# Kernel optimization log

Hardware: AMD Instinct MI355X
Metric: run time of the kernel (lower is better)

The kernel has to match this reference:

```python
import jax, jax.numpy as jnp
import numpy as np

SMOOTHING = 0.9  # NEURON_CONFIG['signal_smoothing']
NUM_SOURCE = 16384
NUM_TARGET = 16384
NUM_BRANCHES = 64
BATCH = 32


def setup_inputs() -> dict:
    key = jax.random.key(0)
    k1, k2, k3, k4 = jax.random.split(key, 4)
    spikes = jax.random.normal(k1, (BATCH, NUM_SOURCE), dtype=jnp.float32)
    attenuation = jax.random.uniform(k2, (NUM_SOURCE, NUM_BRANCHES), dtype=jnp.float32)
    target_indices = jax.random.randint(k3, (NUM_SOURCE, NUM_BRANCHES), 0, NUM_TARGET)
    delays = jax.random.randint(k4, (NUM_SOURCE, NUM_BRANCHES), 0, 6)
    return {"spikes": spikes, "attenuation": attenuation,
            "target_indices": target_indices, "delays": delays}


def reference(spikes, attenuation, target_indices, delays):
    # spikes: [B, S]; attenuation/delays/target_indices: [S, Br]
    B = spikes.shape[0]
    num_target = NUM_TARGET
    att = jnp.clip(attenuation, 0.0, 1.0)
    decay = SMOOTHING ** delays.astype(spikes.dtype)          # [S, Br]
    # fused elementwise: signal per (batch, source, branch)
    signals = spikes[:, :, None] * (att * decay)[None, :, :]   # [B, S, Br]
    flat_t = target_indices.reshape(-1)                        # [S*Br]
    flat_s = signals.reshape(B, -1)                            # [B, S*Br]
    out = jnp.zeros((B, num_target), dtype=spikes.dtype)
    out = out.at[jnp.arange(B)[:, None], flat_t[None, :]].add(flat_s)
    return out
```

## Files before the change

kernel.cpp:

```cpp
#include <hip/hip_runtime.h>

#define S_   16384
#define T_   16384
#define B_   32
#define NEDGES (S_ * 64)
#define GP_  256
#define EPG  4096
#define NBKT 512
#define TPB  32
#define CAP_SRT 2560

__device__ __forceinline__ float edge_weight(float a, int d) {
  float w = fminf(fmaxf(a, 0.0f), 1.0f);
  float r = (d & 1) ? 0.9f : 1.0f;
  r = (d & 2) ? r * 0.81f   : r;
  r = (d & 4) ? r * 0.6561f : r;
  return w * r;
}

__global__ __launch_bounds__(1024) void produce(
    const float* __restrict__ spikes,
    const float* __restrict__ att,
    const int*   __restrict__ tgt,
    const int*   __restrict__ del,
    float*        __restrict__ spikesT,
    int2*         __restrict__ rec,
    unsigned int* __restrict__ ofse) {
  __shared__ float tile[64][33];
  __shared__ int4  sbuf4[EPG / 2];
  __shared__ int   cnt5[NBKT], cur5[NBKT], sofs5[NBKT];
  __shared__ int   wtot[8];
  int2* buf = (int2*)sbuf4;

  const int g   = blockIdx.x;
  const int tid = threadIdx.x;
  if (tid < NBKT) cnt5[tid] = 0;

  const int s0 = g * 64;
  {
    const int x = tid & 63, y = tid >> 6;
    tile[x][y]      = spikes[(size_t)y        * S_ + s0 + x];
    tile[x][y + 16] = spikes[(size_t)(y + 16) * S_ + s0 + x];
  }

  const int e4  = g * 1024 + tid;
  int4   t = reinterpret_cast<const int4*>(tgt)[e4];
  float4 a = reinterpret_cast<const float4*>(att)[e4];
  int4   d = reinterpret_cast<const int4*>(del)[e4];
  const int src = (e4 * 4) >> 6;

  __syncthreads();

  {
    const int b = tid & 31, j = tid >> 5;
    spikesT[(size_t)(s0 + j)      * 32 + b] = tile[j][b];
    spikesT[(size_t)(s0 + j + 32) * 32 + b] = tile[j + 32][b];
  }

  const int bk0 = t.x >> 5, bk1 = t.y >> 5, bk2 = t.z >> 5, bk3 = t.w >> 5;
  __hip_atomic_fetch_add(&cnt5[bk0], 1, __ATOMIC_RELAXED, __HIP_MEMORY_SCOPE_WORKGROUP);
  __hip_atomic_fetch_add(&cnt5[bk1], 1, __ATOMIC_RELAXED, __HIP_MEMORY_SCOPE_WORKGROUP);
  __hip_atomic_fetch_add(&cnt5[bk2], 1, __ATOMIC_RELAXED, __HIP_MEMORY_SCOPE_WORKGROUP);
  __hip_atomic_fetch_add(&cnt5[bk3], 1, __ATOMIC_RELAXED, __HIP_MEMORY_SCOPE_WORKGROUP);
  __syncthreads();

  int v = 0, incl = 0;
  if (tid < NBKT) {
    v = cnt5[tid];
    incl = v;
#pragma unroll
    for (int off = 1; off < 64; off <<= 1) {
      int u = __shfl_up(incl, off);
      if ((tid & 63) >= off) incl += u;
    }
    if ((tid & 63) == 63) wtot[tid >> 6] = incl;
  }
  __syncthreads();
  if (tid < NBKT) {
    int base = 0;
    const int wv = tid >> 6;
    for (int i = 0; i < wv; ++i) base += wtot[i];
    const int start = base + incl - v;
    sofs5[tid] = start;
    cur5[tid]  = start;
  }
  __syncthreads();

#define PUT(BK, TL, AV, DV)                                                   \
  {                                                                           \
    int p = __hip_atomic_fetch_add(&cur5[BK], 1, __ATOMIC_RELAXED,            \
                                   __HIP_MEMORY_SCOPE_WORKGROUP);             \
    buf[p] = make_int2(((TL) << 14) | src,                                    \
                       __float_as_int(edge_weight((AV), (DV))));              \
  }
  PUT(bk0, t.x & 31, a.x, d.x)
  PUT(bk1, t.y & 31, a.y, d.y)
  PUT(bk2, t.z & 31, a.z, d.z)
  PUT(bk3, t.w & 31, a.w, d.w)
#undef PUT
  __syncthreads();

  int4* recO = reinterpret_cast<int4*>(rec) + (size_t)g * (EPG / 2);
  recO[tid]        = sbuf4[tid];
  recO[tid + 1024] = sbuf4[tid + 1024];
  if (tid < NBKT)
    ofse[(size_t)g * NBKT + tid] =
        ((unsigned)cur5[tid] << 16) | (unsigned)sofs5[tid];
}

__global__ __launch_bounds__(512) void consume(
    const int2*  __restrict__ rec,
    const unsigned int* __restrict__ ofse,
    const float* __restrict__ spikesT,
    float* __restrict__ out) {
  __shared__ int2  raw[CAP_SRT];
  __shared__ int2  srt[CAP_SRT];
  __shared__ float otile[TPB][33];
  __shared__ unsigned sse[GP_];
  __shared__ int   sstart[GP_];
  __shared__ int   wtot4[4];
  __shared__ int   h32[TPB], ofs[TPB + 1], cur32[TPB];

  const int k   = blockIdx.x;
  const int tid = threadIdx.x;
  const int b   = tid & 31;
  const int hw  = tid >> 5;

  if (tid < TPB) h32[tid] = 0;
  if (tid < GP_) sse[tid] = ofse[(size_t)tid * NBKT + k];
  __syncthreads();

  int v = 0, incl = 0;
  if (tid < GP_) {
    const unsigned u = sse[tid];
    v = (int)(u >> 16) - (int)(u & 0xFFFF);
    incl = v;
#pragma unroll
    for (int off = 1; off < 64; off <<= 1) {
      int uu = __shfl_up(incl, off);
      if ((tid & 63) >= off) incl += uu;
    }
    if ((tid & 63) == 63) wtot4[tid >> 6] = incl;
  }
  __syncthreads();
  if (tid < GP_) {
    int base = 0;
    const int wv = tid >> 6;
    for (int i = 0; i < wv; ++i) base += wtot4[i];
    sstart[tid] = base + incl - v;
  }
  __syncthreads();
  const int total = min(wtot4[0] + wtot4[1] + wtot4[2] + wtot4[3], CAP_SRT);

  for (int it = 0; it < 16; ++it) {
    const int g = hw + it * 16;
    const unsigned u = sse[g];
    const int st = (int)(u & 0xFFFF);
    const int n  = (int)(u >> 16) - st;
    const int2* slice = rec + (size_t)g * EPG + st;
    const int lbase = sstart[g];
    for (int j = b; j < n; j += 32) {
      int2 r = slice[j];
      __hip_atomic_fetch_add(&h32[(r.x >> 14) & 31], 1, __ATOMIC_RELAXED,
                             __HIP_MEMORY_SCOPE_WORKGROUP);
      const int idx = lbase + j;
      if (idx < CAP_SRT) raw[idx] = r;
    }
  }
  __syncthreads();

  if (tid < 32) {
    int vv = h32[tid], ii = vv;
#pragma unroll
    for (int off = 1; off < 32; off <<= 1) {
      int uu = __shfl_up(ii, off);
      if (tid >= off) ii += uu;
    }
    ofs[tid]   = ii - vv;
    cur32[tid] = ii - vv;
    if (tid == 31) ofs[32] = ii;
  }
  __syncthreads();

  for (int i = tid; i < total; i += 512) {
    int2 r = raw[i];
    int p = __hip_atomic_fetch_add(&cur32[(r.x >> 14) & 31], 1,
                                   __ATOMIC_RELAXED,
                                   __HIP_MEMORY_SCOPE_WORKGROUP);
    if (p < CAP_SRT) srt[p] = r;
  }
  __syncthreads();

  float acc0 = 0.f, acc1 = 0.f;
  {
    int e        = ofs[hw];
    const int e1 = min(ofs[hw + 1], total);
    for (; e + 4 <= e1; e += 4) {
      int2 r0 = srt[e], r1 = srt[e + 1], r2 = srt[e + 2], r3 = srt[e + 3];
      float s0 = spikesT[(size_t)(r0.x & 0x3FFF) * 32 + b];
      float s1 = spikesT[(size_t)(r1.x & 0x3FFF) * 32 + b];
      float s2 = spikesT[(size_t)(r2.x & 0x3FFF) * 32 + b];
      float s3 = spikesT[(size_t)(r3.x & 0x3FFF) * 32 + b];
      acc0 = fmaf(__int_as_float(r0.y), s0, acc0);
      acc0 = fmaf(__int_as_float(r1.y), s1, acc0);
      acc0 = fmaf(__int_as_float(r2.y), s2, acc0);
      acc0 = fmaf(__int_as_float(r3.y), s3, acc0);
    }
    for (; e < e1; ++e) {
      int2 r = srt[e];
      acc0 = fmaf(__int_as_float(r.y), spikesT[(size_t)(r.x & 0x3FFF) * 32 + b], acc0);
    }
  }
  {
    int e        = ofs[hw + 16];
    const int e1 = min(ofs[hw + 17], total);
    for (; e + 4 <= e1; e += 4) {
      int2 r0 = srt[e], r1 = srt[e + 1], r2 = srt[e + 2], r3 = srt[e + 3];
      float s0 = spikesT[(size_t)(r0.x & 0x3FFF) * 32 + b];
      float s1 = spikesT[(size_t)(r1.x & 0x3FFF) * 32 + b];
      float s2 = spikesT[(size_t)(r2.x & 0x3FFF) * 32 + b];
      float s3 = spikesT[(size_t)(r3.x & 0x3FFF) * 32 + b];
      acc1 = fmaf(__int_as_float(r0.y), s0, acc1);
      acc1 = fmaf(__int_as_float(r1.y), s1, acc1);
      acc1 = fmaf(__int_as_float(r2.y), s2, acc1);
      acc1 = fmaf(__int_as_float(r3.y), s3, acc1);
    }
    for (; e < e1; ++e) {
      int2 r = srt[e];
      acc1 = fmaf(__int_as_float(r.y), spikesT[(size_t)(r.x & 0x3FFF) * 32 + b], acc1);
    }
  }

  otile[hw][b]      = acc0;
  otile[hw + 16][b] = acc1;
  __syncthreads();
  const int bb = tid >> 4;
  const int cc = (tid & 15) * 2;
  float2 o2 = make_float2(otile[cc][bb], otile[cc + 1][bb]);
  *reinterpret_cast<float2*>(&out[(size_t)bb * T_ + k * 32 + cc]) = o2;
}

__global__ void zero_floats(float* __restrict__ p, int n) {
  int i = blockIdx.x * blockDim.x + threadIdx.x;
  if (i < n) p[i] = 0.0f;
}

__global__ void naive_kernel(const float* __restrict__ spikes,
                             const float* __restrict__ att,
                             const int*   __restrict__ tgt,
                             const int*   __restrict__ del,
                             float*       __restrict__ out) {
  int i = blockIdx.x * blockDim.x + threadIdx.x;
  if (i >= NEDGES) return;
  int   s = i >> 6;
  int   t = tgt[i];
  float w = edge_weight(att[i], del[i]);
  for (int b = 0; b < B_; ++b)
    unsafeAtomicAdd(&out[(size_t)b * T_ + t], w * spikes[(size_t)b * S_ + s]);
}

extern "C" void kernel_launch(void* const* d_in, const int* in_sizes, int n_in,
                              void* d_out, int out_size, void* d_ws, size_t ws_size,
                              hipStream_t stream) {
  const float* spikes = (const float*)d_in[0];
  const float* att    = (const float*)d_in[1];
  const int*   tgt    = (const int*)d_in[2];
  const int*   del    = (const int*)d_in[3];
  float*       out    = (float*)d_out;

  const size_t spikesT_bytes = (size_t)S_ * B_ * sizeof(float);
  const size_t rec_bytes     = (size_t)NEDGES * sizeof(int2);
  const size_t ofse_bytes    = (size_t)GP_ * NBKT * sizeof(unsigned);
  const size_t need = spikesT_bytes + rec_bytes + ofse_bytes + 64;

  if (ws_size < need) {
    zero_floats<<<(B_ * T_ + 255) / 256, 256, 0, stream>>>(out, B_ * T_);
    naive_kernel<<<(NEDGES + 255) / 256, 256, 0, stream>>>(spikes, att, tgt, del, out);
    return;
  }

  char* p = (char*)d_ws;
  float*        spikesT = (float*)p;        p += spikesT_bytes;
  int2*         rec     = (int2*)p;         p += rec_bytes;
  unsigned int* ofse    = (unsigned int*)p;

  produce<<<GP_, 1024, 0, stream>>>(spikes, att, tgt, del, spikesT, rec, ofse);
  consume<<<NBKT, 512, 0, stream>>>(rec, ofse, spikesT, out);
}
```

Measured before the change: 92.96 us.

## Replace in-block counting sort with shared-memory float atomics in consume

The consume kernel no longer runs a per-block histogram, prefix scan and scatter to group edges by local target. Each half-wave now takes edges straight from the gathered raw buffer in strided order and accumulates weight*spike into a zeroed shared output tile with float atomicAdd. This removes two barriers, the histogram and scatter atomics, and the second shared-memory buffer, which may raise occupancy. In exchange it adds one LDS float atomic per edge per batch lane, and the order of floating-point summation becomes nondeterministic.

```diff
diff --git a/kernel.cpp b/kernel.cpp
--- a/kernel.cpp
+++ b/kernel.cpp
@@ -114,20 +114,18 @@
     const float* __restrict__ spikesT,
     float* __restrict__ out) {
   __shared__ int2  raw[CAP_SRT];
-  __shared__ int2  srt[CAP_SRT];
   __shared__ float otile[TPB][33];
   __shared__ unsigned sse[GP_];
   __shared__ int   sstart[GP_];
   __shared__ int   wtot4[4];
-  __shared__ int   h32[TPB], ofs[TPB + 1], cur32[TPB];
 
   const int k   = blockIdx.x;
   const int tid = threadIdx.x;
   const int b   = tid & 31;
   const int hw  = tid >> 5;
 
-  if (tid < TPB) h32[tid] = 0;
   if (tid < GP_) sse[tid] = ofse[(size_t)tid * NBKT + k];
+  for (int i = tid; i < TPB * 33; i += 512) ((float*)otile)[i] = 0.0f;
   __syncthreads();
 
   int v = 0, incl = 0;
@@ -160,80 +158,33 @@
     const int2* slice = rec + (size_t)g * EPG + st;
     const int lbase = sstart[g];
     for (int j = b; j < n; j += 32) {
-      int2 r = slice[j];
-      __hip_atomic_fetch_add(&h32[(r.x >> 14) & 31], 1, __ATOMIC_RELAXED,
-                             __HIP_MEMORY_SCOPE_WORKGROUP);
       const int idx = lbase + j;
-      if (idx < CAP_SRT) raw[idx] = r;
-    }
-  }
-  __syncthreads();
-
-  if (tid < 32) {
-    int vv = h32[tid], ii = vv;
-#pragma unroll
-    for (int off = 1; off < 32; off <<= 1) {
-      int uu = __shfl_up(ii, off);
-      if (tid >= off) ii += uu;
-    }
-    ofs[tid]   = ii - vv;
-    cur32[tid] = ii - vv;
-    if (tid == 31) ofs[32] = ii;
-  }
-  __syncthreads();
-
-  for (int i = tid; i < total; i += 512) {
-    int2 r = raw[i];
-    int p = __hip_atomic_fetch_add(&cur32[(r.x >> 14) & 31], 1,
-                                   __ATOMIC_RELAXED,
-                                   __HIP_MEMORY_SCOPE_WORKGROUP);
-    if (p < CAP_SRT) srt[p] = r;
-  }
-  __syncthreads();
-
-  float acc0 = 0.f, acc1 = 0.f;
+      if (idx < CAP_SRT) raw[idx] = slice[j];
+    }
+  }
+  __syncthreads();
+
   {
-    int e        = ofs[hw];
-    const int e1 = min(ofs[hw + 1], total);
-    for (; e + 4 <= e1; e += 4) {
-      int2 r0 = srt[e], r1 = srt[e + 1], r2 = srt[e + 2], r3 = srt[e + 3];
+    int i = hw;
+    for (; i + 48 < total; i += 64) {
+      int2 r0 = raw[i], r1 = raw[i + 16], r2 = raw[i + 32], r3 = raw[i + 48];
       float s0 = spikesT[(size_t)(r0.x & 0x3FFF) * 32 + b];
       float s1 = spikesT[(size_t)(r1.x & 0x3FFF) * 32 + b];
       float s2 = spikesT[(size_t)(r2.x & 0x3FFF) * 32 + b];
       float s3 = spikesT[(size_t)(r3.x & 0x3FFF) * 32 + b];
-      acc0 = fmaf(__int_as_float(r0.y), s0, acc0);
-      acc0 = fmaf(__int_as_float(r1.y), s1, acc0);
-      acc0 = fmaf(__int_as_float(r2.y), s2, acc0);
-      acc0 = fmaf(__int_as_float(r3.y), s3, acc0);
-    }
-    for (; e < e1; ++e) {
-      int2 r = srt[e];
-      acc0 = fmaf(__int_as_float(r.y), spikesT[(size_t)(r.x & 0x3FFF) * 32 + b], acc0);
-    }
-  }
-  {
-    int e        = ofs[hw + 16];
-    const int e1 = min(ofs[hw + 17], total);
-    for (; e + 4 <= e1; e += 4) {
-      int2 r0 = srt[e], r1 = srt[e + 1], r2 = srt[e + 2], r3 = srt[e + 3];
-      float s0 = spikesT[(size_t)(r0.x & 0x3FFF) * 32 + b];
-      float s1 = spikesT[(size_t)(r1.x & 0x3FFF) * 32 + b];
-      float s2 = spikesT[(size_t)(r2.x & 0x3FFF) * 32 + b];
-      float s3 = spikesT[(size_t)(r3.x & 0x3FFF) * 32 + b];
-      acc1 = fmaf(__int_as_float(r0.y), s0, acc1);
-      acc1 = fmaf(__int_as_float(r1.y), s1, acc1);
-      acc1 = fmaf(__int_as_float(r2.y), s2, acc1);
-      acc1 = fmaf(__int_as_float(r3.y), s3, acc1);
-    }
-    for (; e < e1; ++e) {
-      int2 r = srt[e];
-      acc1 = fmaf(__int_as_float(r.y), spikesT[(size_t)(r.x & 0x3FFF) * 32 + b], acc1);
-    }
-  }
-
-  otile[hw][b]      = acc0;
-  otile[hw + 16][b] = acc1;
-  __syncthreads();
+      atomicAdd(&otile[(r0.x >> 14) & 31][b], __int_as_float(r0.y) * s0);
+      atomicAdd(&otile[(r1.x >> 14) & 31][b], __int_as_float(r1.y) * s1);
+      atomicAdd(&otile[(r2.x >> 14) & 31][b], __int_as_float(r2.y) * s2);
+      atomicAdd(&otile[(r3.x >> 14) & 31][b], __int_as_float(r3.y) * s3);
+    }
+    for (; i < total; i += 16) {
+      int2 r = raw[i];
+      float s = spikesT[(size_t)(r.x & 0x3FFF) * 32 + b];
+      atomicAdd(&otile[(r.x >> 14) & 31][b], __int_as_float(r.y) * s);
+    }
+  }
+  __syncthreads();
+
   const int bb = tid >> 4;
   const int cc = (tid & 15) * 2;
   float2 o2 = make_float2(otile[cc][bb], otile[cc + 1][bb]);
```

New measurement: 257.0 us. 2.77x slower.
